# Optimization experiments

Hardware: AMD Instinct MI355X
Metric: run time of the kernel (lower is better)

Reference implementation:

```python
import jax, jax.numpy as jnp
import numpy as np

N = 50000      # nodes
E = 800000     # edges (avg degree 16)
F_IN = 128
H = 128
C = 2
EPS = 1e-5


def setup_inputs() -> dict:
    key = jax.random.key(0)
    ks = jax.random.split(key, 16)
    s_in = 1.0 / np.sqrt(F_IN)
    s_h = 1.0 / np.sqrt(H)
    return {
        "x": jax.random.normal(ks[0], (N, F_IN), jnp.float32),
        "edge_index": jax.random.randint(ks[1], (2, E), 0, N, jnp.int32),
        "W1": jax.random.normal(ks[2], (F_IN, H), jnp.float32) * s_in,
        "b1": jnp.zeros((H,), jnp.float32),
        "g1": jax.random.uniform(ks[3], (H,), jnp.float32, 0.5, 1.5),
        "be1": jnp.zeros((H,), jnp.float32),
        "m1": jax.random.normal(ks[4], (H,), jnp.float32) * 0.1,
        "v1": jax.random.uniform(ks[5], (H,), jnp.float32, 0.5, 1.5),
        "W2": jax.random.normal(ks[6], (H, H), jnp.float32) * s_h,
        "b2": jnp.zeros((H,), jnp.float32),
        "g2": jax.random.uniform(ks[7], (H,), jnp.float32, 0.5, 1.5),
        "be2": jnp.zeros((H,), jnp.float32),
        "m2": jax.random.normal(ks[8], (H,), jnp.float32) * 0.1,
        "v2": jax.random.uniform(ks[9], (H,), jnp.float32, 0.5, 1.5),
        "Wc": jax.random.normal(ks[10], (H, C), jnp.float32) * s_h,
        "bc": jnp.zeros((C,), jnp.float32),
    }


def _gcn_norm(edge_index):
    # Add self-loops: A_tilde = A + I, then symmetric normalization D^-1/2 A_tilde D^-1/2.
    loop = jnp.arange(N, dtype=edge_index.dtype)
    src = jnp.concatenate([edge_index[0], loop])
    dst = jnp.concatenate([edge_index[1], loop])
    deg = jax.ops.segment_sum(jnp.ones_like(src, jnp.float32), dst, num_segments=N)
    dinv = jnp.where(deg > 0, jax.lax.rsqrt(jnp.maximum(deg, 1.0)), 0.0)
    norm = dinv[src] * dinv[dst]  # per-edge coefficient
    return src, dst, norm


def _gcn_conv(h, src, dst, norm, W, b):
    h = h @ W                                  # [N, H]
    msg = h[src] * norm[:, None]               # gather + scale, [E+N, H]
    out = jax.ops.segment_sum(msg, dst, num_segments=N)
    return out + b


def _bn_eval(h, g, be, m, v):
    return (h - m) * (g * jax.lax.rsqrt(v + EPS)) + be


def reference(x, edge_index, W1, b1, g1, be1, m1, v1,
              W2, b2, g2, be2, m2, v2, Wc, bc):
    src, dst, norm = _gcn_norm(edge_index)
    h = _gcn_conv(x, src, dst, norm, W1, b1)
    h = jax.nn.relu(_bn_eval(h, g1, be1, m1, v1))  # dropout is identity in eval
    h = _gcn_conv(h, src, dst, norm, W2, b2)
    h = jax.nn.relu(_bn_eval(h, g2, be2, m2, v2))
    return h @ Wc + bc                            # logits [N, 2]
```

## Files before the change

kernel.cpp:

```cpp
#include <hip/hip_runtime.h>
#include <hip/hip_fp16.h>

#define EPSV 1e-5f
#define HSZ 6400
#define BPB 32

using half8 = __attribute__((ext_vector_type(8))) _Float16;
using f32x4 = __attribute__((ext_vector_type(4))) float;

__device__ __forceinline__ int bin_lo(int b, int mul) {
    return (int)((((long long)b << 25) + mul - 1) / mul);
}

__global__ __launch_bounds__(128) void k_setup(const float* __restrict__ W1, const float* __restrict__ W2,
                                               _Float16* __restrict__ whi1, _Float16* __restrict__ wlo1,
                                               _Float16* __restrict__ whi2, _Float16* __restrict__ wlo2,
                                               const float* __restrict__ g1, const float* __restrict__ v1,
                                               const float* __restrict__ b1, const float* __restrict__ m1,
                                               const float* __restrict__ be1,
                                               const float* __restrict__ g2, const float* __restrict__ v2,
                                               const float* __restrict__ b2, const float* __restrict__ m2,
                                               const float* __restrict__ be2,
                                               float* __restrict__ par, int* __restrict__ bcur) {
    int b = blockIdx.x;
    int t = threadIdx.x;
    if (b < 32) {
        const float* W = (b < 16) ? W1 : W2;
        _Float16* whi = (b < 16) ? whi1 : whi2;
        _Float16* wlo = (b < 16) ? wlo1 : wlo2;
        int tile = ((b & 15) << 1) | (t >> 6);
        int l = t & 63;
        int kt = tile >> 3, ct = tile & 7;
        int k0 = kt * 32 + (l >> 4) * 8;
        int c = ct * 16 + (l & 15);
        half8 hi, lo;
#pragma unroll
        for (int j = 0; j < 8; j++) {
            float w = W[(k0 + j) * 128 + c];
            _Float16 h = (_Float16)w;
            hi[j] = h;
            lo[j] = (_Float16)(w - (float)h);
        }
        size_t o = (size_t)tile * 64 + l;
        ((half8*)whi)[o] = hi;
        ((half8*)wlo)[o] = lo;
    } else {
        int c = t;
        float s1 = g1[c] * rsqrtf(v1[c] + EPSV);
        par[c] = s1;
        par[128 + c] = fmaf(b1[c] - m1[c], s1, be1[c]);
        float s2 = g2[c] * rsqrtf(v2[c] + EPSV);
        par[256 + c] = s2;
        par[384 + c] = fmaf(b2[c] - m2[c], s2, be2[c]);
        if (c < 8) bcur[c] = 0;
    }
}

__device__ __forceinline__ void bin_body(const int* __restrict__ src, const int* __restrict__ dst,
                                         int* __restrict__ bcur, unsigned int* __restrict__ binned,
                                         int E, int mul, int bin_cap, int bid, int nblocks, int tid) {
    int lane = tid & 63;
    int gw = (bid * 256 + tid) >> 6;
    int nw = (nblocks * 256) >> 6;
    bool v4 = ((E & 3) == 0);
    for (int base = gw * 1024; base < E; base += nw * 1024) {
        unsigned int vals[16];
        int bins[16];
        unsigned long long clo = 0, chi = 0;
#pragma unroll
        for (int g = 0; g < 4; g++) {
            int e0 = base + g * 256 + lane * 4;
            int4 s4, d4;
            if (v4 && e0 + 3 < E) {
                s4 = *(const int4*)(src + e0);
                d4 = *(const int4*)(dst + e0);
            } else {
                s4.x = (e0 < E) ? src[e0] : 0;         d4.x = (e0 < E) ? dst[e0] : -1;
                s4.y = (e0 + 1 < E) ? src[e0 + 1] : 0; d4.y = (e0 + 1 < E) ? dst[e0 + 1] : -1;
                s4.z = (e0 + 2 < E) ? src[e0 + 2] : 0; d4.z = (e0 + 2 < E) ? dst[e0 + 2] : -1;
                s4.w = (e0 + 3 < E) ? src[e0 + 3] : 0; d4.w = (e0 + 3 < E) ? dst[e0 + 3] : -1;
            }
            int ss[4] = {s4.x, s4.y, s4.z, s4.w};
            int dd[4] = {d4.x, d4.y, d4.z, d4.w};
#pragma unroll
            for (int k = 0; k < 4; k++) {
                int j = g * 4 + k;
                int d = dd[k];
                if (d >= 0) {
                    vals[j] = ((unsigned int)ss[k] << 16) | (unsigned int)d;
                    int b = (d * mul) >> 25;
                    bins[j] = b;
                    if (b < 4) clo += 1ull << (b * 16);
                    else       chi += 1ull << ((b - 4) * 16);
                } else bins[j] = -1;
            }
        }
        unsigned long long ilo = clo, ihi = chi;
#pragma unroll
        for (int d = 1; d < 64; d <<= 1) {
            unsigned long long ulo = __shfl_up(ilo, d, 64);
            unsigned long long uhi = __shfl_up(ihi, d, 64);
            if (lane >= d) { ilo += ulo; ihi += uhi; }
        }
        unsigned long long tlo = __shfl(ilo, 63, 64), thi = __shfl(ihi, 63, 64);
        unsigned long long plo = ilo - clo, phi = ihi - chi;
        int mytot = 0;
        if (lane < 4) mytot = (int)((tlo >> (lane * 16)) & 0xffff);
        else if (lane < 8) mytot = (int)((thi >> ((lane - 4) * 16)) & 0xffff);
        int alloc = 0;
        if (lane < 8) alloc = atomicAdd(&bcur[lane], mytot);
#pragma unroll
        for (int j = 0; j < 16; j++) {
            int b = bins[j];
            int bs = (b < 0) ? 0 : b;
            int bbase = __shfl(alloc, bs, 64);
            int sh = (bs & 3) * 16;
            unsigned long long sel = (bs < 4) ? plo : phi;
            int rel = (int)((sel >> sh) & 0xffffu);
            unsigned long long inc = 1ull << sh;
            if (bs < 4) plo += inc; else phi += inc;
            if (b >= 0) binned[(size_t)bs * bin_cap + bbase + rel] = vals[j];
        }
    }
}

template <bool AFP16>
__device__ __forceinline__ void gemm_body(const void* __restrict__ Araw,
                                          const _Float16* __restrict__ whi,
                                          const _Float16* __restrict__ wlo,
                                          unsigned short* __restrict__ out, int M,
                                          int bid, int tid, uint4* __restrict__ sB) {
    int l = tid & 63;
    int w = tid >> 6;
    int r0 = bid * 64 + w * 16;
    int ra = r0 + (l & 15);
    if (ra >= M) ra = M - 1;
    int kl = (l >> 4) * 8;

    half8 avh[4];
    float4 af0[4], af1[4];
    if constexpr (AFP16) {
#pragma unroll
        for (int kt = 0; kt < 4; kt++)
            avh[kt] = *(const half8*)((const _Float16*)Araw + (size_t)ra * 128 + kt * 32 + kl);
    } else {
#pragma unroll
        for (int kt = 0; kt < 4; kt++) {
            const float* pa = (const float*)Araw + (size_t)ra * 128 + kt * 32 + kl;
            af0[kt] = *(const float4*)pa;
            af1[kt] = *(const float4*)(pa + 4);
        }
    }

    {
        const uint4* gh = (const uint4*)whi;
        const uint4* gl = (const uint4*)wlo;
#pragma unroll
        for (int i = 0; i < 8; i++) sB[tid + i * 256] = gh[tid + i * 256];
#pragma unroll
        for (int i = 0; i < 8; i++) sB[2048 + tid + i * 256] = gl[tid + i * 256];
    }
    __syncthreads();

    f32x4 acc[8];
#pragma unroll
    for (int i = 0; i < 8; i++) acc[i] = (f32x4)0.f;

    const half8* bh8 = (const half8*)sB;
    const half8* bl8 = (const half8*)(sB + 2048);

#pragma unroll
    for (int kt = 0; kt < 4; kt++) {
        half8 ah, al;
        if constexpr (AFP16) {
            ah = avh[kt];
        } else {
            float fa[8] = {af0[kt].x, af0[kt].y, af0[kt].z, af0[kt].w,
                           af1[kt].x, af1[kt].y, af1[kt].z, af1[kt].w};
#pragma unroll
            for (int j = 0; j < 8; j++) {
                _Float16 h = (_Float16)fa[j];
                ah[j] = h;
                al[j] = (_Float16)(fa[j] - (float)h);
            }
        }
#pragma unroll
        for (int ct = 0; ct < 8; ct++) {
            half8 bh = bh8[(kt * 8 + ct) * 64 + l];
            half8 bl = bl8[(kt * 8 + ct) * 64 + l];
            acc[ct] = __builtin_amdgcn_mfma_f32_16x16x32_f16(ah, bh, acc[ct], 0, 0, 0);
            if constexpr (!AFP16)
                acc[ct] = __builtin_amdgcn_mfma_f32_16x16x32_f16(al, bh, acc[ct], 0, 0, 0);
            acc[ct] = __builtin_amdgcn_mfma_f32_16x16x32_f16(ah, bl, acc[ct], 0, 0, 0);
        }
    }

    __syncthreads();
    _Float16* stw = (_Float16*)sB + w * 2048;
#pragma unroll
    for (int r = 0; r < 4; r++) {
        int trow = (l >> 4) * 4 + r;
#pragma unroll
        for (int ct = 0; ct < 8; ct++)
            stw[trow * 128 + ct * 16 + (l & 15)] = (_Float16)(acc[ct][r]);
    }
#pragma unroll
    for (int p = 0; p < 4; p++) {
        int trow = p * 4 + (l >> 4);
        int grow = r0 + trow;
        if (grow < M) {
            uint4 v = *(const uint4*)&stw[trow * 128 + (l & 15) * 8];
            *(uint4*)&out[(size_t)grow * 128 + (l & 15) * 8] = v;
        }
    }
}

__global__ __launch_bounds__(256) void k_bingemm(const int* __restrict__ src, const int* __restrict__ dst,
                                                 int* __restrict__ bcur, unsigned int* __restrict__ binned,
                                                 int E, int mul, int bin_cap,
                                                 const float* __restrict__ x,
                                                 const _Float16* __restrict__ whi,
                                                 const _Float16* __restrict__ wlo,
                                                 unsigned short* __restrict__ outHs, int M, int bin_blocks) {
    __shared__ uint4 sB[4096];
    if ((int)blockIdx.x < bin_blocks) {
        bin_body(src, dst, bcur, binned, E, mul, bin_cap, blockIdx.x, bin_blocks, threadIdx.x);
        return;
    }
    gemm_body<false>(x, whi, wlo, outHs, M, blockIdx.x - bin_blocks, threadIdx.x, sB);
}

template <bool AFP16>
__global__ __launch_bounds__(256) void k_gemm(const void* __restrict__ Araw,
                                              const _Float16* __restrict__ whi,
                                              const _Float16* __restrict__ wlo,
                                              unsigned short* __restrict__ out, int M) {
    __shared__ uint4 sB[4096];
    gemm_body<AFP16>(Araw, whi, wlo, out, M, blockIdx.x, threadIdx.x, sB);
}

__global__ __launch_bounds__(256) void k_count(const unsigned int* __restrict__ binned,
                                               const int* __restrict__ bcnt, int* __restrict__ phist,
                                               int mul, int bin_cap) {
    __shared__ int hist[HSZ];
    int b = blockIdx.x & 7;
    int blk = blockIdx.x >> 3;
    int t = threadIdx.x;
    for (int i = t; i < HSZ; i += 256) hist[i] = 0;
    __syncthreads();
    int lo = bin_lo(b, mul);
    int cnt = bcnt[b];
    int e0 = (int)((long long)blk * cnt / BPB);
    int e1 = (int)((long long)(blk + 1) * cnt / BPB);
    const unsigned int* bp = binned + (size_t)b * bin_cap;
    for (int i = e0 + t; i < e1; i += 256) {
        int d = (int)(bp[i] & 0xffffu);
        atomicAdd(&hist[d - lo], 1);
    }
    __syncthreads();
    int* ph = phist + (size_t)blockIdx.x * HSZ;
    for (int i = t; i < HSZ; i += 256) ph[i] = hist[i];
}

__global__ __launch_bounds__(256) void k_bsum(int* __restrict__ phist, int* __restrict__ deg,
                                              int* __restrict__ bsum, int N, int mul) {
    int t = threadIdx.x;
    int base = blockIdx.x * 1024;
    int s = 0;
    for (int j = 0; j < 4; j++) {
        int i = base + j * 256 + t;
        if (i < N) {
            int b = (i * mul) >> 25;
            int lo = bin_lo(b, mul);
            int local = i - lo;
            int run = 0;
#pragma unroll
            for (int blk = 0; blk < BPB; blk++) {
                int* p = phist + (size_t)(blk * 8 + b) * HSZ + local;
                int c = *p;
                *p = run;
                run += c;
            }
            deg[i] = run;
            s += (run + 7) & ~7;
        }
    }
#pragma unroll
    for (int d = 1; d < 64; d <<= 1) s += __shfl_xor(s, d, 64);
    __shared__ int ws[4];
    if ((t & 63) == 0) ws[t >> 6] = s;
    __syncthreads();
    if (t == 0) bsum[blockIdx.x] = ws[0] + ws[1] + ws[2] + ws[3];
}

__global__ __launch_bounds__(256) void k_scanout(const int* __restrict__ deg, const int* __restrict__ bsum,
                                                 int* __restrict__ row_start, int* __restrict__ rend,
                                                 float* __restrict__ dinv, int n, int nb) {
    __shared__ int s_boff;
    __shared__ int ws[4];
    int t = threadIdx.x, lane = t & 63, wid = t >> 6;
    if (t < 64) {
        int v = (t < nb) ? bsum[t] : 0;
        int incl = v;
#pragma unroll
        for (int d = 1; d < 64; d <<= 1) {
            int u = __shfl_up(incl, d, 64);
            if (t >= d) incl += u;
        }
        if (t == (int)blockIdx.x) s_boff = incl - v;
    }
    __syncthreads();
    int base = blockIdx.x * 1024 + t * 4;
    int v[4], pv[4], ts = 0;
#pragma unroll
    for (int j = 0; j < 4; j++) {
        v[j] = (base + j < n) ? deg[base + j] : 0;
        pv[j] = (v[j] + 7) & ~7;
        ts += pv[j];
    }
    int incl = ts;
#pragma unroll
    for (int d = 1; d < 64; d <<= 1) {
        int u = __shfl_up(incl, d, 64);
        if (lane >= d) incl += u;
    }
    if (lane == 63) ws[wid] = incl;
    __syncthreads();
    int wo = 0;
    for (int i = 0; i < wid; i++) wo += ws[i];
    int run = s_boff + wo + (incl - ts);
#pragma unroll
    for (int j = 0; j < 4; j++) {
        if (base + j < n) {
            row_start[base + j] = run;
            rend[base + j] = run + v[j];
            dinv[base + j] = rsqrtf((float)v[j] + 1.0f);
            run += pv[j];
        }
    }
}

__global__ __launch_bounds__(256) void k_fill(const unsigned int* __restrict__ binned,
                                              const int* __restrict__ bcnt, const int* __restrict__ row_start,
                                              const int* __restrict__ phist, const float* __restrict__ dinv,
                                              unsigned int* __restrict__ csr,
                                              int N, int mul, int bin_cap) {
    __shared__ int cur[HSZ];
    int b = blockIdx.x & 7;
    int blk = blockIdx.x >> 3;
    int t = threadIdx.x;
    int lo = bin_lo(b, mul);
    int hi = (b == 7) ? N : bin_lo(b + 1, mul);
    if (hi > N) hi = N;
    const int* ph = phist + (size_t)blockIdx.x * HSZ;
    for (int i = t; i < HSZ; i += 256) {
        int d = lo + i;
        cur[i] = (d < hi) ? (row_start[d] + ph[i]) : 0;
    }
    __syncthreads();
    int cnt = bcnt[b];
    int e0 = (int)((long long)blk * cnt / BPB);
    int e1 = (int)((long long)(blk + 1) * cnt / BPB);
    const unsigned int* bp = binned + (size_t)b * bin_cap;
    for (int i = e0 + t; i < e1; i += 256) {
        unsigned int v = bp[i];
        int d = (int)(v & 0xffffu);
        int s = (int)(v >> 16);
        __half h = __float2half_rn(dinv[s]);
        unsigned short hb = *(unsigned short*)&h;
        int q = atomicAdd(&cur[d - lo], 1);
        csr[q] = ((unsigned int)hb << 16) | (unsigned int)s;
    }
}

__device__ __forceinline__ void f2fma(float2& a, const __half2 h, float w) {
    float2 f = __half22float2(h);
    a.x = fmaf(f.x, w, a.x);
    a.y = fmaf(f.y, w, a.y);
}

__device__ __forceinline__ float pk_w(unsigned int pk) {
    __half h;
    *(unsigned short*)&h = (unsigned short)(pk >> 16);
    return __half2float(h);
}

__device__ __forceinline__ void aggr_gather(const float4* __restrict__ Hs4, const unsigned int* __restrict__ csr,
                                            int rs, int re, int node, float dn, int lc, float2 acc[4]) {
    {
        float4 sv = Hs4[(size_t)node * 16 + lc];
        const __half2* h = (const __half2*)&sv;
        float2 f0 = __half22float2(h[0]), f1 = __half22float2(h[1]);
        float2 f2 = __half22float2(h[2]), f3 = __half22float2(h[3]);
        acc[0] = make_float2(f0.x * dn, f0.y * dn);
        acc[1] = make_float2(f1.x * dn, f1.y * dn);
        acc[2] = make_float2(f2.x * dn, f2.y * dn);
        acc[3] = make_float2(f3.x * dn, f3.y * dn);
    }
    int nch = (re - rs + 7) >> 3;
    if (nch <= 0) return;
    float2 accB[4] = {{0.f, 0.f}, {0.f, 0.f}, {0.f, 0.f}, {0.f, 0.f}};
    const uint4* cp = (const uint4*)(csr + rs);
    uint4 qa0 = cp[0], qa1 = cp[1];
    uint4 qb0 = cp[2], qb1 = cp[3];
    for (int c = 0; c < nch; c += 2) {
        uint4 na0 = qa0, na1 = qa1, nb0 = qb0, nb1 = qb1;
        if (c + 2 < nch) { na0 = cp[2 * c + 4]; na1 = cp[2 * c + 5]; nb0 = cp[2 * c + 6]; nb1 = cp[2 * c + 7]; }
        unsigned int pA[8] = {qa0.x, qa0.y, qa0.z, qa0.w, qa1.x, qa1.y, qa1.z, qa1.w};
        unsigned int pB[8] = {qb0.x, qb0.y, qb0.z, qb0.w, qb1.x, qb1.y, qb1.z, qb1.w};
        int baseA = rs + c * 8;
        int baseB = baseA + 8;
        float4 vA[8], vB[8];
        float wA[8], wB[8];
#pragma unroll
        for (int j = 0; j < 8; j++) {
            unsigned int pk = (baseA + j < re) ? pA[j] : 0u;
            wA[j] = pk_w(pk);
            vA[j] = Hs4[(size_t)(pk & 0xffffu) * 16 + lc];
        }
#pragma unroll
        for (int j = 0; j < 8; j++) {
            unsigned int pk = (baseB + j < re) ? pB[j] : 0u;
            wB[j] = pk_w(pk);
            vB[j] = Hs4[(size_t)(pk & 0xffffu) * 16 + lc];
        }
#pragma unroll
        for (int j = 0; j < 8; j++) {
            const __half2* h = (const __half2*)&vA[j];
            float2* acp = (j & 1) ? accB : acc;
            f2fma(acp[0], h[0], wA[j]);
            f2fma(acp[1], h[1], wA[j]);
            f2fma(acp[2], h[2], wA[j]);
            f2fma(acp[3], h[3], wA[j]);
        }
#pragma unroll
        for (int j = 0; j < 8; j++) {
            const __half2* h = (const __half2*)&vB[j];
            float2* acp = (j & 1) ? accB : acc;
            f2fma(acp[0], h[0], wB[j]);
            f2fma(acp[1], h[1], wB[j]);
            f2fma(acp[2], h[2], wB[j]);
            f2fma(acp[3], h[3], wB[j]);
        }
        qa0 = na0; qa1 = na1; qb0 = nb0; qb1 = nb1;
    }
#pragma unroll
    for (int k = 0; k < 4; k++) {
        acc[k].x += accB[k].x;
        acc[k].y += accB[k].y;
    }
}

__device__ __forceinline__ void bn_relu(const float2 acc[4], float dn, const float* __restrict__ par,
                                        int lc, float4& y0, float4& y1) {
    float4 s0 = ((const float4*)par)[lc * 2];
    float4 s1 = ((const float4*)par)[lc * 2 + 1];
    float4 t0 = ((const float4*)par)[32 + lc * 2];
    float4 t1 = ((const float4*)par)[32 + lc * 2 + 1];
    y0.x = fmaxf(fmaf(acc[0].x * dn, s0.x, t0.x), 0.f);
    y0.y = fmaxf(fmaf(acc[0].y * dn, s0.y, t0.y), 0.f);
    y0.z = fmaxf(fmaf(acc[1].x * dn, s0.z, t0.z), 0.f);
    y0.w = fmaxf(fmaf(acc[1].y * dn, s0.w, t0.w), 0.f);
    y1.x = fmaxf(fmaf(acc[2].x * dn, s1.x, t1.x), 0.f);
    y1.y = fmaxf(fmaf(acc[2].y * dn, s1.y, t1.y), 0.f);
    y1.z = fmaxf(fmaf(acc[3].x * dn, s1.z, t1.z), 0.f);
    y1.w = fmaxf(fmaf(acc[3].y * dn, s1.w, t1.w), 0.f);
}

__global__ __launch_bounds__(256) void k_aggr(const float4* __restrict__ Hs4, const int* __restrict__ row_start,
                                              const int* __restrict__ rend,
                                              const unsigned int* __restrict__ csr, const float* __restrict__ dinv,
                                              const float* __restrict__ par, uint4* __restrict__ out, int n) {
    int lc = threadIdx.x & 15;
    int node = blockIdx.x * 16 + (threadIdx.x >> 4);
    if (node >= n) return;
    float dn = dinv[node];
    float2 acc[4];
    aggr_gather(Hs4, csr, row_start[node], rend[node], node, dn, lc, acc);
    float4 y0, y1;
    bn_relu(acc, dn, par, lc, y0, y1);
    __half2 p0 = __floats2half2_rn(y0.x, y0.y);
    __half2 p1 = __floats2half2_rn(y0.z, y0.w);
    __half2 p2 = __floats2half2_rn(y1.x, y1.y);
    __half2 p3 = __floats2half2_rn(y1.z, y1.w);
    uint4 pk;
    pk.x = *(unsigned int*)&p0;
    pk.y = *(unsigned int*)&p1;
    pk.z = *(unsigned int*)&p2;
    pk.w = *(unsigned int*)&p3;
    out[(size_t)node * 16 + lc] = pk;
}

__global__ __launch_bounds__(256) void k_aggr_cls(const float4* __restrict__ Hs4, const int* __restrict__ row_start,
                                                  const int* __restrict__ rend,
                                                  const unsigned int* __restrict__ csr, const float* __restrict__ dinv,
                                                  const float* __restrict__ par, const float4* __restrict__ Wc4,
                                                  const float* __restrict__ bc, float2* __restrict__ out, int n) {
    int lc = threadIdx.x & 15;
    int node = blockIdx.x * 16 + (threadIdx.x >> 4);
    if (node >= n) return;
    float dn = dinv[node];
    float2 acc[4];
    aggr_gather(Hs4, csr, row_start[node], rend[node], node, dn, lc, acc);
    float4 y0, y1;
    bn_relu(acc, dn, par, lc, y0, y1);
    float4 w0 = Wc4[lc * 4], w1 = Wc4[lc * 4 + 1], w2 = Wc4[lc * 4 + 2], w3 = Wc4[lc * 4 + 3];
    float p0 = y0.x * w0.x + y0.y * w0.z + y0.z * w1.x + y0.w * w1.z
             + y1.x * w2.x + y1.y * w2.z + y1.z * w3.x + y1.w * w3.z;
    float p1 = y0.x * w0.y + y0.y * w0.w + y0.z * w1.y + y0.w * w1.w
             + y1.x * w2.y + y1.y * w2.w + y1.z * w3.y + y1.w * w3.w;
#pragma unroll
    for (int d = 1; d < 16; d <<= 1) {
        p0 += __shfl_xor(p0, d, 16);
        p1 += __shfl_xor(p1, d, 16);
    }
    if (lc == 0) out[node] = make_float2(p0 + bc[0], p1 + bc[1]);
}

extern "C" void kernel_launch(void* const* d_in, const int* in_sizes, int n_in,
                              void* d_out, int out_size, void* d_ws, size_t ws_size,
                              hipStream_t stream) {
    const float* x = (const float*)d_in[0];
    const int* ei = (const int*)d_in[1];
    const float* W1 = (const float*)d_in[2];
    const float* b1 = (const float*)d_in[3];
    const float* g1 = (const float*)d_in[4];
    const float* be1 = (const float*)d_in[5];
    const float* m1 = (const float*)d_in[6];
    const float* v1 = (const float*)d_in[7];
    const float* W2 = (const float*)d_in[8];
    const float* b2 = (const float*)d_in[9];
    const float* g2 = (const float*)d_in[10];
    const float* be2 = (const float*)d_in[11];
    const float* m2 = (const float*)d_in[12];
    const float* v2 = (const float*)d_in[13];
    const float* Wc = (const float*)d_in[14];
    const float* bc = (const float*)d_in[15];
    float* out = (float*)d_out;

    const int N = in_sizes[0] / 128;
    const int E = in_sizes[1] / 2;
    const int* src = ei;
    const int* dst = ei + E;

    const int mul = (int)((8LL << 25) / N);
    const int bin_cap = ((E / 8 + 8192 + 63) / 64) * 64;

    int* W = (int*)d_ws;
    size_t off = 0;
    int* deg = W + off; off += N;
    int* bcur = W + off; off += 8;
    int* row_start = W + off; off += (size_t)N + 1;
    int* rend = W + off; off += N;
    float* dinv = (float*)(W + off); off += N;
    int* bsum = W + off; off += 64;
    float* par = (float*)(W + off); off += 512;
    _Float16* whi1 = (_Float16*)(W + off); off += 8192;
    _Float16* wlo1 = (_Float16*)(W + off); off += 8192;
    _Float16* whi2 = (_Float16*)(W + off); off += 8192;
    _Float16* wlo2 = (_Float16*)(W + off); off += 8192;
    int* phist = W + off; off += (size_t)8 * BPB * HSZ;
    unsigned int* csr = (unsigned int*)(W + off); off += (size_t)E + 8 * N + 64;
    unsigned int* binned = (unsigned int*)(W + off); off += (size_t)8 * bin_cap;
    off = (off + 3) & ~(size_t)3;
    __half* Hs = (__half*)(W + off); off += (size_t)N * 64;
    _Float16* Ag = (_Float16*)(W + off);

    k_setup<<<33, 128, 0, stream>>>(W1, W2, whi1, wlo1, whi2, wlo2,
                                    g1, v1, b1, m1, be1, g2, v2, b2, m2, be2,
                                    par, bcur);

    int nb = (N + 1023) / 1024;
    int gbm = (N + 63) / 64;
    int bin_blocks = 512;
    k_bingemm<<<bin_blocks + gbm, 256, 0, stream>>>(src, dst, bcur, binned, E, mul, bin_cap,
                                                    x, whi1, wlo1, (unsigned short*)Hs, N, bin_blocks);
    k_count<<<8 * BPB, 256, 0, stream>>>(binned, bcur, phist, mul, bin_cap);
    k_bsum<<<nb, 256, 0, stream>>>(phist, deg, bsum, N, mul);
    k_scanout<<<nb, 256, 0, stream>>>(deg, bsum, row_start, rend, dinv, N, nb);
    k_fill<<<8 * BPB, 256, 0, stream>>>(binned, bcur, row_start, phist, dinv, csr, N, mul, bin_cap);

    int ab = (N + 15) / 16;
    k_aggr<<<ab, 256, 0, stream>>>((const float4*)Hs, row_start, rend, csr, dinv, par, (uint4*)Ag, N);
    k_gemm<true><<<gbm, 256, 0, stream>>>(Ag, whi2, wlo2, (unsigned short*)Hs, N);
    k_aggr_cls<<<ab, 256, 0, stream>>>((const float4*)Hs, row_start, rend, csr, dinv, par + 256,
                                       (const float4*)Wc, bc, (float2*)out, N);
}
```

Baseline: 149.1 us.

## Fuse layer-1 aggregation with layer-2 GEMM in one block kernel

Replaces the separate layer-1 aggregation kernel and layer-2 GEMM kernel with one kernel. Each 1024-thread block aggregates 64 nodes, applies BN+ReLU, stages the fp16 rows in padded shared memory, and runs the MFMA GEMM against W2 (hi/lo split) before writing to a new buffer. The gather also changes to process 8 neighbours per chunk with two accumulators and prefetched CSR entries. This removes one launch and the global round trip of the intermediate activations. The cost is a large block with heavy shared-memory use, which may lower occupancy, and the GEMM has to wait for the slowest node's gather in each block.

Result: no change. 149.0 us (-0.1%).

```diff
diff --git a/kernel.cpp b/kernel.cpp
--- a/kernel.cpp
+++ b/kernel.cpp
@@ -124,12 +124,11 @@
     }
 }
 
-template <bool AFP16>
-__device__ __forceinline__ void gemm_body(const void* __restrict__ Araw,
-                                          const _Float16* __restrict__ whi,
-                                          const _Float16* __restrict__ wlo,
-                                          unsigned short* __restrict__ out, int M,
-                                          int bid, int tid, uint4* __restrict__ sB) {
+__device__ __forceinline__ void gemm_body_f32(const float* __restrict__ A,
+                                              const _Float16* __restrict__ whi,
+                                              const _Float16* __restrict__ wlo,
+                                              unsigned short* __restrict__ out, int M,
+                                              int bid, int tid, uint4* __restrict__ sB) {
     int l = tid & 63;
     int w = tid >> 6;
     int r0 = bid * 64 + w * 16;
@@ -137,19 +136,12 @@
     if (ra >= M) ra = M - 1;
     int kl = (l >> 4) * 8;
 
-    half8 avh[4];
     float4 af0[4], af1[4];
-    if constexpr (AFP16) {
-#pragma unroll
-        for (int kt = 0; kt < 4; kt++)
-            avh[kt] = *(const half8*)((const _Float16*)Araw + (size_t)ra * 128 + kt * 32 + kl);
-    } else {
-#pragma unroll
-        for (int kt = 0; kt < 4; kt++) {
-            const float* pa = (const float*)Araw + (size_t)ra * 128 + kt * 32 + kl;
-            af0[kt] = *(const float4*)pa;
-            af1[kt] = *(const float4*)(pa + 4);
-        }
+#pragma unroll
+    for (int kt = 0; kt < 4; kt++) {
+        const float* pa = A + (size_t)ra * 128 + kt * 32 + kl;
+        af0[kt] = *(const float4*)pa;
+        af1[kt] = *(const float4*)(pa + 4);
     }
 
     {
@@ -172,25 +164,20 @@
 #pragma unroll
     for (int kt = 0; kt < 4; kt++) {
         half8 ah, al;
-        if constexpr (AFP16) {
-            ah = avh[kt];
-        } else {
-            float fa[8] = {af0[kt].x, af0[kt].y, af0[kt].z, af0[kt].w,
-                           af1[kt].x, af1[kt].y, af1[kt].z, af1[kt].w};
-#pragma unroll
-            for (int j = 0; j < 8; j++) {
-                _Float16 h = (_Float16)fa[j];
-                ah[j] = h;
-                al[j] = (_Float16)(fa[j] - (float)h);
-            }
+        float fa[8] = {af0[kt].x, af0[kt].y, af0[kt].z, af0[kt].w,
+                       af1[kt].x, af1[kt].y, af1[kt].z, af1[kt].w};
+#pragma unroll
+        for (int j = 0; j < 8; j++) {
+            _Float16 h = (_Float16)fa[j];
+            ah[j] = h;
+            al[j] = (_Float16)(fa[j] - (float)h);
         }
 #pragma unroll
         for (int ct = 0; ct < 8; ct++) {
             half8 bh = bh8[(kt * 8 + ct) * 64 + l];
             half8 bl = bl8[(kt * 8 + ct) * 64 + l];
             acc[ct] = __builtin_amdgcn_mfma_f32_16x16x32_f16(ah, bh, acc[ct], 0, 0, 0);
-            if constexpr (!AFP16)
-                acc[ct] = __builtin_amdgcn_mfma_f32_16x16x32_f16(al, bh, acc[ct], 0, 0, 0);
+            acc[ct] = __builtin_amdgcn_mfma_f32_16x16x32_f16(al, bh, acc[ct], 0, 0, 0);
             acc[ct] = __builtin_amdgcn_mfma_f32_16x16x32_f16(ah, bl, acc[ct], 0, 0, 0);
         }
     }
@@ -227,16 +214,7 @@
         bin_body(src, dst, bcur, binned, E, mul, bin_cap, blockIdx.x, bin_blocks, threadIdx.x);
         return;
     }
-    gemm_body<false>(x, whi, wlo, outHs, M, blockIdx.x - bin_blocks, threadIdx.x, sB);
-}
-
-template <bool AFP16>
-__global__ __launch_bounds__(256) void k_gemm(const void* __restrict__ Araw,
-                                              const _Float16* __restrict__ whi,
-                                              const _Float16* __restrict__ wlo,
-                                              unsigned short* __restrict__ out, int M) {
-    __shared__ uint4 sB[4096];
-    gemm_body<AFP16>(Araw, whi, wlo, out, M, blockIdx.x, threadIdx.x, sB);
+    gemm_body_f32(x, whi, wlo, outHs, M, blockIdx.x - bin_blocks, threadIdx.x, sB);
 }
 
 __global__ __launch_bounds__(256) void k_count(const unsigned int* __restrict__ binned,
@@ -385,8 +363,157 @@
     return __half2float(h);
 }
 
-__device__ __forceinline__ void aggr_gather(const float4* __restrict__ Hs4, const unsigned int* __restrict__ csr,
-                                            int rs, int re, int node, float dn, int lc, float2 acc[4]) {
+__device__ __forceinline__ void aggr_gather1(const float4* __restrict__ Hs4, const unsigned int* __restrict__ csr,
+                                             int rs, int re, int node, float dn, int lc, float2 acc[4]) {
+    {
+        float4 sv = Hs4[(size_t)node * 16 + lc];
+        const __half2* h = (const __half2*)&sv;
+        float2 f0 = __half22float2(h[0]), f1 = __half22float2(h[1]);
+        float2 f2 = __half22float2(h[2]), f3 = __half22float2(h[3]);
+        acc[0] = make_float2(f0.x * dn, f0.y * dn);
+        acc[1] = make_float2(f1.x * dn, f1.y * dn);
+        acc[2] = make_float2(f2.x * dn, f2.y * dn);
+        acc[3] = make_float2(f3.x * dn, f3.y * dn);
+    }
+    int nch = (re - rs + 7) >> 3;
+    if (nch <= 0) return;
+    float2 accB[4] = {{0.f, 0.f}, {0.f, 0.f}, {0.f, 0.f}, {0.f, 0.f}};
+    const uint4* cp = (const uint4*)(csr + rs);
+    uint4 q0 = cp[0], q1 = cp[1];
+    for (int c = 0; c < nch; c++) {
+        uint4 n0 = q0, n1 = q1;
+        if (c + 1 < nch) { n0 = cp[2 * c + 2]; n1 = cp[2 * c + 3]; }
+        unsigned int pks[8] = {q0.x, q0.y, q0.z, q0.w, q1.x, q1.y, q1.z, q1.w};
+        int base = rs + c * 8;
+        float4 v[8];
+        float w[8];
+#pragma unroll
+        for (int j = 0; j < 8; j++) {
+            unsigned int pk = (base + j < re) ? pks[j] : 0u;
+            w[j] = pk_w(pk);
+            v[j] = Hs4[(size_t)(pk & 0xffffu) * 16 + lc];
+        }
+#pragma unroll
+        for (int j = 0; j < 8; j++) {
+            const __half2* h = (const __half2*)&v[j];
+            float2* acp = (j & 1) ? accB : acc;
+            f2fma(acp[0], h[0], w[j]);
+            f2fma(acp[1], h[1], w[j]);
+            f2fma(acp[2], h[2], w[j]);
+            f2fma(acp[3], h[3], w[j]);
+        }
+        q0 = n0; q1 = n1;
+    }
+#pragma unroll
+    for (int k = 0; k < 4; k++) {
+        acc[k].x += accB[k].x;
+        acc[k].y += accB[k].y;
+    }
+}
+
+__device__ __forceinline__ void bn_relu(const float2 acc[4], float dn, const float* __restrict__ par,
+                                        int lc, float4& y0, float4& y1) {
+    float4 s0 = ((const float4*)par)[lc * 2];
+    float4 s1 = ((const float4*)par)[lc * 2 + 1];
+    float4 t0 = ((const float4*)par)[32 + lc * 2];
+    float4 t1 = ((const float4*)par)[32 + lc * 2 + 1];
+    y0.x = fmaxf(fmaf(acc[0].x * dn, s0.x, t0.x), 0.f);
+    y0.y = fmaxf(fmaf(acc[0].y * dn, s0.y, t0.y), 0.f);
+    y0.z = fmaxf(fmaf(acc[1].x * dn, s0.z, t0.z), 0.f);
+    y0.w = fmaxf(fmaf(acc[1].y * dn, s0.w, t0.w), 0.f);
+    y1.x = fmaxf(fmaf(acc[2].x * dn, s1.x, t1.x), 0.f);
+    y1.y = fmaxf(fmaf(acc[2].y * dn, s1.y, t1.y), 0.f);
+    y1.z = fmaxf(fmaf(acc[3].x * dn, s1.z, t1.z), 0.f);
+    y1.w = fmaxf(fmaf(acc[3].y * dn, s1.w, t1.w), 0.f);
+}
+
+#define APAD 136
+__global__ __launch_bounds__(1024, 4) void k_aggr_gemm(const float4* __restrict__ Hs4,
+                                                       const int* __restrict__ row_start,
+                                                       const int* __restrict__ rend,
+                                                       const unsigned int* __restrict__ csr,
+                                                       const float* __restrict__ dinv,
+                                                       const float* __restrict__ par,
+                                                       const _Float16* __restrict__ whi,
+                                                       const _Float16* __restrict__ wlo,
+                                                       unsigned short* __restrict__ outHs2, int n) {
+    __shared__ uint4 sB[4096];
+    __shared__ _Float16 sA[64 * APAD];
+    int t = threadIdx.x;
+
+    {
+        const uint4* gh = (const uint4*)whi;
+        const uint4* gl = (const uint4*)wlo;
+        sB[t] = gh[t];
+        sB[t + 1024] = gh[t + 1024];
+        sB[t + 2048] = gl[t];
+        sB[t + 3072] = gl[t + 1024];
+    }
+
+    int lc = t & 15;
+    int nl = t >> 4;
+    int node = blockIdx.x * 64 + nl;
+    float4 y0 = make_float4(0.f, 0.f, 0.f, 0.f);
+    float4 y1 = make_float4(0.f, 0.f, 0.f, 0.f);
+    if (node < n) {
+        float dn = dinv[node];
+        float2 acc[4];
+        aggr_gather1(Hs4, csr, row_start[node], rend[node], node, dn, lc, acc);
+        bn_relu(acc, dn, par, lc, y0, y1);
+    }
+    {
+        half8 av;
+        av[0] = (_Float16)y0.x; av[1] = (_Float16)y0.y; av[2] = (_Float16)y0.z; av[3] = (_Float16)y0.w;
+        av[4] = (_Float16)y1.x; av[5] = (_Float16)y1.y; av[6] = (_Float16)y1.z; av[7] = (_Float16)y1.w;
+        *(half8*)&sA[nl * APAD + lc * 8] = av;
+    }
+    __syncthreads();
+
+    int w = t >> 6, l = t & 63;
+    const half8* bh8 = (const half8*)sB;
+    const half8* bl8 = (const half8*)(sB + 2048);
+    f32x4 accT[2];
+#pragma unroll
+    for (int tt = 0; tt < 2; tt++) {
+        int tile = w * 2 + tt;
+        int rt = tile >> 3, ct = tile & 7;
+        f32x4 acc = (f32x4)0.f;
+#pragma unroll
+        for (int kt = 0; kt < 4; kt++) {
+            half8 a = *(const half8*)&sA[(rt * 16 + (l & 15)) * APAD + kt * 32 + (l >> 4) * 8];
+            half8 bh = bh8[(kt * 8 + ct) * 64 + l];
+            half8 bl = bl8[(kt * 8 + ct) * 64 + l];
+            acc = __builtin_amdgcn_mfma_f32_16x16x32_f16(a, bh, acc, 0, 0, 0);
+            acc = __builtin_amdgcn_mfma_f32_16x16x32_f16(a, bl, acc, 0, 0, 0);
+        }
+        accT[tt] = acc;
+    }
+    __syncthreads();
+
+#pragma unroll
+    for (int tt = 0; tt < 2; tt++) {
+        int tile = w * 2 + tt;
+        int rt = tile >> 3, ct = tile & 7;
+#pragma unroll
+        for (int r = 0; r < 4; r++) {
+            int row = rt * 16 + (l >> 4) * 4 + r;
+            sA[row * APAD + ct * 16 + (l & 15)] = (_Float16)(accT[tt][r]);
+        }
+    }
+    __syncthreads();
+
+    {
+        int row = t >> 4;
+        int grow = blockIdx.x * 64 + row;
+        if (grow < n) {
+            uint4 v = *(const uint4*)&sA[row * APAD + (t & 15) * 8];
+            *(uint4*)&outHs2[(size_t)grow * 128 + (t & 15) * 8] = v;
+        }
+    }
+}
+
+__device__ __forceinline__ void aggr_gather2(const float4* __restrict__ Hs4, const unsigned int* __restrict__ csr,
+                                             int rs, int re, int node, float dn, int lc, float2 acc[4]) {
     {
         float4 sv = Hs4[(size_t)node * 16 + lc];
         const __half2* h = (const __half2*)&sv;
@@ -451,46 +578,6 @@
     }
 }
 
-__device__ __forceinline__ void bn_relu(const float2 acc[4], float dn, const float* __restrict__ par,
-                                        int lc, float4& y0, float4& y1) {
-    float4 s0 = ((const float4*)par)[lc * 2];
-    float4 s1 = ((const float4*)par)[lc * 2 + 1];
-    float4 t0 = ((const float4*)par)[32 + lc * 2];
-    float4 t1 = ((const float4*)par)[32 + lc * 2 + 1];
-    y0.x = fmaxf(fmaf(acc[0].x * dn, s0.x, t0.x), 0.f);
-    y0.y = fmaxf(fmaf(acc[0].y * dn, s0.y, t0.y), 0.f);
-    y0.z = fmaxf(fmaf(acc[1].x * dn, s0.z, t0.z), 0.f);
-    y0.w = fmaxf(fmaf(acc[1].y * dn, s0.w, t0.w), 0.f);
-    y1.x = fmaxf(fmaf(acc[2].x * dn, s1.x, t1.x), 0.f);
-    y1.y = fmaxf(fmaf(acc[2].y * dn, s1.y, t1.y), 0.f);
-    y1.z = fmaxf(fmaf(acc[3].x * dn, s1.z, t1.z), 0.f);
-    y1.w = fmaxf(fmaf(acc[3].y * dn, s1.w, t1.w), 0.f);
-}
-
-__global__ __launch_bounds__(256) void k_aggr(const float4* __restrict__ Hs4, const int* __restrict__ row_start,
-                                              const int* __restrict__ rend,
-                                              const unsigned int* __restrict__ csr, const float* __restrict__ dinv,
-                                              const float* __restrict__ par, uint4* __restrict__ out, int n) {
-    int lc = threadIdx.x & 15;
-    int node = blockIdx.x * 16 + (threadIdx.x >> 4);
-    if (node >= n) return;
-    float dn = dinv[node];
-    float2 acc[4];
-    aggr_gather(Hs4, csr, row_start[node], rend[node], node, dn, lc, acc);
-    float4 y0, y1;
-    bn_relu(acc, dn, par, lc, y0, y1);
-    __half2 p0 = __floats2half2_rn(y0.x, y0.y);
-    __half2 p1 = __floats2half2_rn(y0.z, y0.w);
-    __half2 p2 = __floats2half2_rn(y1.x, y1.y);
-    __half2 p3 = __floats2half2_rn(y1.z, y1.w);
-    uint4 pk;
-    pk.x = *(unsigned int*)&p0;
-    pk.y = *(unsigned int*)&p1;
-    pk.z = *(unsigned int*)&p2;
-    pk.w = *(unsigned int*)&p3;
-    out[(size_t)node * 16 + lc] = pk;
-}
-
 __global__ __launch_bounds__(256) void k_aggr_cls(const float4* __restrict__ Hs4, const int* __restrict__ row_start,
                                                   const int* __restrict__ rend,
                                                   const unsigned int* __restrict__ csr, const float* __restrict__ dinv,
@@ -501,7 +588,7 @@
     if (node >= n) return;
     float dn = dinv[node];
     float2 acc[4];
-    aggr_gather(Hs4, csr, row_start[node], rend[node], node, dn, lc, acc);
+    aggr_gather2(Hs4, csr, row_start[node], rend[node], node, dn, lc, acc);
     float4 y0, y1;
     bn_relu(acc, dn, par, lc, y0, y1);
     float4 w0 = Wc4[lc * 4], w1 = Wc4[lc * 4 + 1], w2 = Wc4[lc * 4 + 2], w3 = Wc4[lc * 4 + 3];
@@ -564,7 +651,7 @@
     unsigned int* binned = (unsigned int*)(W + off); off += (size_t)8 * bin_cap;
     off = (off + 3) & ~(size_t)3;
     __half* Hs = (__half*)(W + off); off += (size_t)N * 64;
-    _Float16* Ag = (_Float16*)(W + off);
+    __half* Hs2 = (__half*)(W + off);
 
     k_setup<<<33, 128, 0, stream>>>(W1, W2, whi1, wlo1, whi2, wlo2,
                                     g1, v1, b1, m1, be1, g2, v2, b2, m2, be2,
@@ -580,9 +667,9 @@
     k_scanout<<<nb, 256, 0, stream>>>(deg, bsum, row_start, rend, dinv, N, nb);
     k_fill<<<8 * BPB, 256, 0, stream>>>(binned, bcur, row_start, phist, dinv, csr, N, mul, bin_cap);
 
+    k_aggr_gemm<<<gbm, 1024, 0, stream>>>((const float4*)Hs, row_start, rend, csr, dinv, par,
+                                          whi2, wlo2, (unsigned short*)Hs2, N);
     int ab = (N + 15) / 16;
-    k_aggr<<<ab, 256, 0, stream>>>((const float4*)Hs, row_start, rend, csr, dinv, par, (uint4*)Ag, N);
-    k_gemm<true><<<gbm, 256, 0, stream>>>(Ag, whi2, wlo2, (unsigned short*)Hs, N);
-    k_aggr_cls<<<ab, 256, 0, stream>>>((const float4*)Hs, row_start, rend, csr, dinv, par + 256,
+    k_aggr_cls<<<ab, 256, 0, stream>>>((const float4*)Hs2, row_start, rend, csr, dinv, par + 256,
                                        (const float4*)Wc, bc, (float2*)out, N);
 }
```
